# Kernel tuning notes

Hardware: AMD Instinct MI355X
Metric: run time of the kernel (lower is better)

## Reference

```python
import jax, jax.numpy as jnp
import numpy as np

L, S = 3, 5                 # A hierarchy layers, subsets per layer
CIN = COUT = 64
INTER = COUT // (S - 1)     # 16
BC = COUT // 4              # 16 channels per TCN branch
N, T, V = 128, 128, 25
KS = 5
DILS = (1, 2)
EPS = 1e-5


def setup_inputs() -> dict:
    key = jax.random.key(0)
    ks = jax.random.split(key, 22)
    rn = lambda i, shape, s=0.1: jax.random.normal(ks[i], shape, jnp.float32) * s
    g1 = lambda i, shape: 1.0 + jax.random.normal(ks[i], shape, jnp.float32) * 0.05
    return {
        'x':      jax.random.normal(ks[0], (N, CIN, T, V), jnp.float32),
        'PA':     rn(1, (L, S, V, V), 0.2),
        'gdw':    rn(2, (L, INTER, CIN)),
        'gdb':    rn(3, (L, INTER)),
        'gdg':    g1(4, (L, INTER)),
        'gdbt':   rn(5, (L, INTER)),
        'gsw':    rn(6, (L, S, INTER, INTER)),
        'gsb':    rn(7, (L, S, INTER)),
        'gsg':    g1(8, (L, S, INTER)),
        'gsbt':   rn(9, (L, S, INTER)),
        'gbng':   g1(10, (COUT,)),
        'gbnb':   rn(11, (COUT,)),
        'brw':    rn(12, (4, BC, COUT)),
        'brb':    rn(13, (4, BC)),
        'brg':    g1(14, (4, BC)),
        'brbt':   rn(15, (4, BC)),
        'tcw':    rn(16, (2, BC, BC, KS, 1)),
        'tcbias': rn(17, (2, BC)),
        'tcg':    g1(18, (2, BC)),
        'tcbt':   rn(19, (2, BC)),
        'mpg':    g1(20, (BC,)),
        'mpb':    rn(21, (BC,)),
    }


def _bn(x, g, b):
    # training-mode BatchNorm2d over (N, T, V) with biased variance
    m = x.mean(axis=(0, 2, 3), keepdims=True)
    v = ((x - m) ** 2).mean(axis=(0, 2, 3), keepdims=True)
    return (x - m) * jax.lax.rsqrt(v + EPS) * g[None, :, None, None] + b[None, :, None, None]


def _c1x1(x, w, b=None):
    y = jnp.einsum('nctv,oc->notv', x, w)
    return y if b is None else y + b[None, :, None, None]


def reference(x, PA, gdw, gdb, gdg, gdbt, gsw, gsb, gsg, gsbt, gbng, gbnb,
              brw, brb, brg, brbt, tcw, tcbias, tcg, tcbt, mpg, mpb):
    # ---- UbH_Gconv ----
    layer_outs = []
    for i in range(L):
        xd = jax.nn.relu(_bn(_c1x1(x, gdw[i], gdb[i]), gdg[i], gdbt[i]))
        ys = [
            _bn(_c1x1(jnp.einsum('nctu,vu->nctv', xd, PA[i, j]), gsw[i, j], gsb[i, j]),
                gsg[i, j], gsbt[i, j])
            for j in range(S)
        ]
        layer_outs.append(jnp.concatenate(ys, axis=1))      # [N, S*INTER, T, V]
    out = jnp.stack(layer_outs, axis=2)                     # [N, S*INTER, L, T, V]
    base = out[:, :INTER]                                   # subset-0 block
    new = out[:, INTER:] + jnp.tile(base, (1, S - 1, 1, 1, 1))
    new = new.sum(axis=2)                                   # sum over hierarchy layers -> [N, COUT, T, V]
    xg = jax.nn.relu(_bn(new, gbng, gbnb) + x)              # residual down is identity (CIN==COUT)

    # ---- MultiScale_TemporalConv (residual=False) ----
    branches = []
    for k, d in enumerate(DILS):
        y = jax.nn.relu(_bn(_c1x1(xg, brw[k], brb[k]), brg[k], brbt[k]))
        pad = (KS + (KS - 1) * (d - 1) - 1) // 2
        y = jax.lax.conv_general_dilated(
            y, tcw[k], window_strides=(1, 1), padding=((pad, pad), (0, 0)),
            rhs_dilation=(d, 1), dimension_numbers=('NCHW', 'OIHW', 'NCHW'))
        y = y + tcbias[k][None, :, None, None]
        branches.append(_bn(y, tcg[k], tcbt[k]))
    # maxpool branch
    y = jax.nn.relu(_bn(_c1x1(xg, brw[2], brb[2]), brg[2], brbt[2]))
    y = jax.lax.reduce_window(y, -jnp.inf, jax.lax.max, (1, 1, 3, 1), (1, 1, 1, 1),
                              ((0, 0), (0, 0), (1, 1), (0, 0)))
    branches.append(_bn(y, mpg, mpb))
    # plain 1x1 branch
    branches.append(_bn(_c1x1(xg, brw[3], brb[3]), brg[3], brbt[3]))

    t = jnp.concatenate(branches, axis=1)                   # [N, COUT, T, V]
    # unit residual is identity (CIN==COUT, stride==1)
    return jax.nn.relu(t + xg)
```

## Files before the change

kernel.cpp:

```cpp
#include <hip/hip_runtime.h>

#define N_ 128
#define T_ 128
#define V_ 25
#define TV 3200
#define LL 3
#define SS 5
#define II 16
#define EPSB 1e-5f
#define MCNT 409600.0f


__device__ __forceinline__ float2 bncoef(const float2* st, int slot, float g, float bt){
  float2 s = st[slot];
  float m  = s.x * (1.0f/MCNT);
  float var = s.y * (1.0f/MCNT) - m*m;
  float a = g * rsqrtf(var + EPSB);
  return make_float2(a, bt - m*a);
}

__global__ __launch_bounds__(256) void k1_conv_dw(
    const float* __restrict__ x, const float* __restrict__ gdw, const float* __restrict__ gdb,
    float* __restrict__ c1, float2* st)
{
  __shared__ float w[64*48];
  __shared__ float bias[48];
  __shared__ float bst[4][96];
  const int tid = threadIdx.x;
  for (int i = tid; i < 64*48; i += 256){ int c = i/48, o = i - c*48; w[i] = gdw[o*64 + c]; }
  if (tid < 48) bias[tid] = gdb[tid];
  __syncthreads();
  const int n = blockIdx.y;
  const int rem = blockIdx.x*256 + tid;
  const bool act = rem < TV;
  float acc[48];
  #pragma unroll
  for (int o = 0; o < 48; o++) acc[o] = act ? bias[o] : 0.f;
  const float* xp = x + (size_t)n*64*TV + rem;
  if (act){
    #pragma unroll 4
    for (int c = 0; c < 64; c++){
      float xv = xp[c*TV];
      const float4* w4 = (const float4*)&w[c*48];
      #pragma unroll
      for (int o4 = 0; o4 < 12; o4++){
        float4 ww = w4[o4];
        acc[o4*4+0] += ww.x*xv; acc[o4*4+1] += ww.y*xv;
        acc[o4*4+2] += ww.z*xv; acc[o4*4+3] += ww.w*xv;
      }
    }
    #pragma unroll
    for (int o = 0; o < 48; o++){
      int l = o >> 4, oi = o & 15;
      c1[(size_t)((l*N_+n)*II + oi)*TV + rem] = acc[o];
    }
  }
  const int wv = tid >> 6, lane = tid & 63;
  #pragma unroll
  for (int o = 0; o < 48; o++){
    float s = acc[o], q = acc[o]*acc[o];
    #pragma unroll
    for (int m = 32; m; m >>= 1){ s += __shfl_xor(s, m); q += __shfl_xor(q, m); }
    if (lane == 0){ bst[wv][2*o] = s; bst[wv][2*o+1] = q; }
  }
  __syncthreads();
  float* stf = (float*)st;
  if (tid < 96) unsafeAtomicAdd(stf + tid, bst[0][tid]+bst[1][tid]+bst[2][tid]+bst[3][tid]);
}

__global__ __launch_bounds__(256) void k2_spatial_stats(
    const float* __restrict__ c1, const float* __restrict__ PA,
    const float* __restrict__ gsw, const float* __restrict__ gsb,
    const float* __restrict__ gdg, const float* __restrict__ gdbt,
    float2* st)
{
  __shared__ float pa[5][25][28];
  __shared__ float gw[5][16][20];
  __shared__ float xdl[4][16][28];
  __shared__ float zz[4][25][20];
  __shared__ float cA[16], cB[16];
  __shared__ float bst[4][160];
  const int tid = threadIdx.x;
  const int l = blockIdx.z, n = blockIdx.y;
  for (int i = tid; i < 5*625; i += 256){ int j = i/625, r = i - j*625; pa[j][r/25][r%25] = PA[(l*5+j)*625 + r]; }
  for (int i = tid; i < 5*256; i += 256){ int j = i >> 8, r = i & 255; gw[j][r>>4][r&15] = gsw[(l*5+j)*256 + r]; }
  if (tid < 16){
    float2 ab = bncoef(st, l*16+tid, gdg[l*16+tid], gdbt[l*16+tid]);
    cA[tid] = ab.x; cB[tid] = ab.y;
  }
  __syncthreads();
  const int wv = tid >> 6, lane = tid & 63, oc = lane & 15, vg = lane >> 4;
  const int t = blockIdx.x*4 + wv;
  const float* c1p = c1 + (size_t)((l*N_+n)*II)*TV + t*25;
  for (int idx = lane; idx < 400; idx += 64){
    int c = idx/25, v = idx - c*25;
    float val = c1p[c*TV + v];
    xdl[wv][c][v] = fmaxf(cA[c]*val + cB[c], 0.f);
  }
  float xdr[25];
  {
    const float4* xr4 = (const float4*)&xdl[wv][oc][0];
    #pragma unroll
    for (int u4 = 0; u4 < 6; u4++){
      float4 x4 = xr4[u4];
      xdr[u4*4+0]=x4.x; xdr[u4*4+1]=x4.y; xdr[u4*4+2]=x4.z; xdr[u4*4+3]=x4.w;
    }
    xdr[24] = xdl[wv][oc][24];
  }
  #pragma unroll 1
  for (int j = 0; j < 5; j++){
    #pragma unroll
    for (int k = 0; k < 7; k++){
      int v = vg + 4*k;
      if (v < 25){
        const float4* p4 = (const float4*)&pa[j][v][0];
        float zv = 0.f;
        #pragma unroll
        for (int u4 = 0; u4 < 6; u4++){
          float4 pp = p4[u4];
          zv += xdr[u4*4+0]*pp.x + xdr[u4*4+1]*pp.y + xdr[u4*4+2]*pp.z + xdr[u4*4+3]*pp.w;
        }
        zv += xdr[24]*pa[j][v][24];
        zz[wv][v][oc] = zv;
      }
    }
    float gwr[16];
    {
      const float4* g4 = (const float4*)&gw[j][oc][0];
      #pragma unroll
      for (int c4 = 0; c4 < 4; c4++){
        float4 gg = g4[c4];
        gwr[c4*4+0]=gg.x; gwr[c4*4+1]=gg.y; gwr[c4*4+2]=gg.z; gwr[c4*4+3]=gg.w;
      }
    }
    const float bjo = gsb[(l*5+j)*16 + oc];
    float s = 0.f, q = 0.f;
    #pragma unroll
    for (int k = 0; k < 7; k++){
      int v = vg + 4*k;
      if (v < 25){
        const float4* z4 = (const float4*)&zz[wv][v][0];
        float cv = bjo;
        #pragma unroll
        for (int c4 = 0; c4 < 4; c4++){
          float4 zf = z4[c4];
          cv += gwr[c4*4+0]*zf.x + gwr[c4*4+1]*zf.y + gwr[c4*4+2]*zf.z + gwr[c4*4+3]*zf.w;
        }
        s += cv; q += cv*cv;
      }
    }
    s += __shfl_xor(s,16); s += __shfl_xor(s,32);
    q += __shfl_xor(q,16); q += __shfl_xor(q,32);
    if (vg == 0){ bst[wv][2*(j*16+oc)] = s; bst[wv][2*(j*16+oc)+1] = q; }
  }
  __syncthreads();
  float* stf = (float*)st;
  for (int i = tid; i < 160; i += 256)
    unsafeAtomicAdd(stf + 96 + l*160 + i, bst[0][i]+bst[1][i]+bst[2][i]+bst[3][i]);
}

__global__ __launch_bounds__(256) void k3_new(
    const float* __restrict__ c1, const float* __restrict__ PA,
    const float* __restrict__ gsw, const float* __restrict__ gsb,
    const float* __restrict__ gdg, const float* __restrict__ gdbt,
    const float* __restrict__ gsg, const float* __restrict__ gsbt,
    float2* st, float* __restrict__ newb)
{
  __shared__ float pa[5][25][28];
  __shared__ float gw[5][16][20];
  __shared__ float xdl[4][16][28];
  __shared__ float zz[4][25][20];
  __shared__ float cA[16], cB[16];
  __shared__ float c2A[5][16], c2B[5][16];
  __shared__ float bst[4][128];
  const int tid = threadIdx.x;
  const int n = blockIdx.y;
  const int wv = tid >> 6, lane = tid & 63, oc = lane & 15, vg = lane >> 4;
  const int t = blockIdx.x*4 + wv;
  float base[7], ac1[7], ac2[7], ac3[7], ac4[7];
  #pragma unroll
  for (int k = 0; k < 7; k++){ base[k]=0.f; ac1[k]=0.f; ac2[k]=0.f; ac3[k]=0.f; ac4[k]=0.f; }

  #pragma unroll 1
  for (int l = 0; l < 3; l++){
    __syncthreads();
    for (int i = tid; i < 5*625; i += 256){ int j = i/625, r = i - j*625; pa[j][r/25][r%25] = PA[(l*5+j)*625 + r]; }
    for (int i = tid; i < 5*256; i += 256){ int j = i >> 8, r = i & 255; gw[j][r>>4][r&15] = gsw[(l*5+j)*256 + r]; }
    if (tid < 16){
      float2 ab = bncoef(st, l*16+tid, gdg[l*16+tid], gdbt[l*16+tid]);
      cA[tid] = ab.x; cB[tid] = ab.y;
    }
    if (tid < 80){
      int j = tid >> 4, o = tid & 15;
      float2 ab = bncoef(st, 48 + (l*5+j)*16 + o, gsg[(l*5+j)*16+o], gsbt[(l*5+j)*16+o]);
      c2A[j][o] = ab.x; c2B[j][o] = ab.y;
    }
    __syncthreads();
    const float* c1p = c1 + (size_t)((l*N_+n)*II)*TV + t*25;
    for (int idx = lane; idx < 400; idx += 64){
      int c = idx/25, v = idx - c*25;
      float val = c1p[c*TV + v];
      xdl[wv][c][v] = fmaxf(cA[c]*val + cB[c], 0.f);
    }
    float xdr[25];
    {
      const float4* xr4 = (const float4*)&xdl[wv][oc][0];
      #pragma unroll
      for (int u4 = 0; u4 < 6; u4++){
        float4 x4 = xr4[u4];
        xdr[u4*4+0]=x4.x; xdr[u4*4+1]=x4.y; xdr[u4*4+2]=x4.z; xdr[u4*4+3]=x4.w;
      }
      xdr[24] = xdl[wv][oc][24];
    }
    #pragma unroll 1
    for (int j = 0; j < 5; j++){
      #pragma unroll
      for (int k = 0; k < 7; k++){
        int v = vg + 4*k;
        if (v < 25){
          const float4* p4 = (const float4*)&pa[j][v][0];
          float zv = 0.f;
          #pragma unroll
          for (int u4 = 0; u4 < 6; u4++){
            float4 pp = p4[u4];
            zv += xdr[u4*4+0]*pp.x + xdr[u4*4+1]*pp.y + xdr[u4*4+2]*pp.z + xdr[u4*4+3]*pp.w;
          }
          zv += xdr[24]*pa[j][v][24];
          zz[wv][v][oc] = zv;
        }
      }
      float gwr[16];
      {
        const float4* g4 = (const float4*)&gw[j][oc][0];
        #pragma unroll
        for (int c4 = 0; c4 < 4; c4++){
          float4 gg = g4[c4];
          gwr[c4*4+0]=gg.x; gwr[c4*4+1]=gg.y; gwr[c4*4+2]=gg.z; gwr[c4*4+3]=gg.w;
        }
      }
      const float bjo = gsb[(l*5+j)*16 + oc];
      const float a2 = c2A[j][oc], b2 = c2B[j][oc];
      float ybuf[7];
      #pragma unroll
      for (int k = 0; k < 7; k++){
        int v = vg + 4*k;
        ybuf[k] = 0.f;
        if (v < 25){
          const float4* z4 = (const float4*)&zz[wv][v][0];
          float cv = bjo;
          #pragma unroll
          for (int c4 = 0; c4 < 4; c4++){
            float4 zf = z4[c4];
            cv += gwr[c4*4+0]*zf.x + gwr[c4*4+1]*zf.y + gwr[c4*4+2]*zf.z + gwr[c4*4+3]*zf.w;
          }
          ybuf[k] = a2*cv + b2;
        }
      }
      if (j == 0){
        #pragma unroll
        for (int k = 0; k < 7; k++) base[k] += ybuf[k];
      } else if (j == 1){
        #pragma unroll
        for (int k = 0; k < 7; k++) ac1[k] += ybuf[k];
      } else if (j == 2){
        #pragma unroll
        for (int k = 0; k < 7; k++) ac2[k] += ybuf[k];
      } else if (j == 3){
        #pragma unroll
        for (int k = 0; k < 7; k++) ac3[k] += ybuf[k];
      } else {
        #pragma unroll
        for (int k = 0; k < 7; k++) ac4[k] += ybuf[k];
      }
    }
  }
  float* np = newb + (size_t)n*64*TV + t*25;
  float s0=0.f,q0=0.f,s1=0.f,q1=0.f,s2=0.f,q2=0.f,s3=0.f,q3=0.f;
  #pragma unroll
  for (int k = 0; k < 7; k++){
    int v = vg + 4*k;
    if (v < 25){
      float v0 = ac1[k] + base[k];
      float v1 = ac2[k] + base[k];
      float v2 = ac3[k] + base[k];
      float v3 = ac4[k] + base[k];
      np[(0*16+oc)*TV + v] = v0;
      np[(1*16+oc)*TV + v] = v1;
      np[(2*16+oc)*TV + v] = v2;
      np[(3*16+oc)*TV + v] = v3;
      s0 += v0; q0 += v0*v0;
      s1 += v1; q1 += v1*v1;
      s2 += v2; q2 += v2*v2;
      s3 += v3; q3 += v3*v3;
    }
  }
  s0 += __shfl_xor(s0,16); s0 += __shfl_xor(s0,32);
  q0 += __shfl_xor(q0,16); q0 += __shfl_xor(q0,32);
  s1 += __shfl_xor(s1,16); s1 += __shfl_xor(s1,32);
  q1 += __shfl_xor(q1,16); q1 += __shfl_xor(q1,32);
  s2 += __shfl_xor(s2,16); s2 += __shfl_xor(s2,32);
  q2 += __shfl_xor(q2,16); q2 += __shfl_xor(q2,32);
  s3 += __shfl_xor(s3,16); s3 += __shfl_xor(s3,32);
  q3 += __shfl_xor(q3,16); q3 += __shfl_xor(q3,32);
  if (vg == 0){
    bst[wv][2*(0*16+oc)] = s0; bst[wv][2*(0*16+oc)+1] = q0;
    bst[wv][2*(1*16+oc)] = s1; bst[wv][2*(1*16+oc)+1] = q1;
    bst[wv][2*(2*16+oc)] = s2; bst[wv][2*(2*16+oc)+1] = q2;
    bst[wv][2*(3*16+oc)] = s3; bst[wv][2*(3*16+oc)+1] = q3;
  }
  __syncthreads();
  float* stf = (float*)st;
  for (int i = tid; i < 128; i += 256)
    unsafeAtomicAdd(stf + 576 + i, bst[0][i]+bst[1][i]+bst[2][i]+bst[3][i]);
}

__global__ __launch_bounds__(256) void k4_xg_branches(
    const float* __restrict__ x, const float* __restrict__ newb,
    const float* __restrict__ gbng, const float* __restrict__ gbnb,
    const float* __restrict__ brw, const float* __restrict__ brb,
    float2* st, float* __restrict__ xg, float* __restrict__ y)
{
  __shared__ float w[64*64];
  __shared__ float cA[64], cB[64], bias[64];
  __shared__ float bst[4][128];
  const int tid = threadIdx.x;
  for (int i = tid; i < 4096; i += 256){ int c = i >> 6, ko = i & 63; w[i] = brw[ko*64 + c]; }
  if (tid < 64){
    float2 ab = bncoef(st, 288+tid, gbng[tid], gbnb[tid]);
    cA[tid] = ab.x; cB[tid] = ab.y; bias[tid] = brb[tid];
  }
  __syncthreads();
  const int n = blockIdx.y;
  const int rem = blockIdx.x*256 + tid;
  const bool act = rem < TV;
  const float* xp  = x    + (size_t)n*64*TV + rem;
  const float* npx = newb + (size_t)n*64*TV + rem;
  float*       xgp = xg   + (size_t)n*64*TV + rem;
  float xgv[64];
  #pragma unroll
  for (int c = 0; c < 64; c++){
    float v = 0.f;
    if (act){
      v = fmaxf(cA[c]*npx[c*TV] + cB[c] + xp[c*TV], 0.f);
      xgp[c*TV] = v;
    }
    xgv[c] = v;
  }
  const int wv = tid >> 6, lane = tid & 63;
  #pragma unroll
  for (int k = 0; k < 4; k++){
    float acc[16];
    #pragma unroll
    for (int o = 0; o < 16; o++) acc[o] = act ? bias[k*16+o] : 0.f;
    #pragma unroll
    for (int c = 0; c < 64; c++){
      float xv = xgv[c];
      const float4* w4 = (const float4*)&w[c*64 + k*16];
      #pragma unroll
      for (int o4 = 0; o4 < 4; o4++){
        float4 ww = w4[o4];
        acc[o4*4+0] += ww.x*xv; acc[o4*4+1] += ww.y*xv;
        acc[o4*4+2] += ww.z*xv; acc[o4*4+3] += ww.w*xv;
      }
    }
    if (act){
      float* yp = y + (size_t)((k*N_+n)*16)*TV + rem;
      #pragma unroll
      for (int o = 0; o < 16; o++) yp[o*TV] = acc[o];
    }
    #pragma unroll
    for (int o = 0; o < 16; o++){
      float s = acc[o], q = acc[o]*acc[o];
      #pragma unroll
      for (int m = 32; m; m >>= 1){ s += __shfl_xor(s, m); q += __shfl_xor(q, m); }
      if (lane == 0){ bst[wv][2*(k*16+o)] = s; bst[wv][2*(k*16+o)+1] = q; }
    }
  }
  __syncthreads();
  float* stf = (float*)st;
  for (int i = tid; i < 128; i += 256)
    unsafeAtomicAdd(stf + 704 + i, bst[0][i]+bst[1][i]+bst[2][i]+bst[3][i]);
}

__global__ __launch_bounds__(256) void k5_temporal(
    const float* __restrict__ y, const float* __restrict__ tcw, const float* __restrict__ tcbias,
    const float* __restrict__ brg, const float* __restrict__ brbt,
    float2* st, float* __restrict__ tp)
{
  __shared__ float wt[2*16*5*16];
  __shared__ float cAy[48], cBy[48];
  __shared__ float bst[4][96];
  const int tid = threadIdx.x;
  for (int i = tid; i < 2560; i += 256){
    int k = i/1280, r = i - k*1280, c = r/80, r2 = r - c*80, ks = r2 >> 4, o = r2 & 15;
    wt[i] = tcw[((k*16+o)*16 + c)*5 + ks];
  }
  if (tid < 48){
    float2 ab = bncoef(st, 352+tid, brg[tid], brbt[tid]);
    cAy[tid] = ab.x; cBy[tid] = ab.y;
  }
  __syncthreads();
  const int n = blockIdx.y;
  const int rem = blockIdx.x*256 + tid;
  const bool act = rem < TV;
  const int t = rem/25, v = rem - t*25;
  const int wv = tid >> 6, lane = tid & 63;
  #pragma unroll
  for (int k = 0; k < 2; k++){
    const int d = k + 1;
    float acc[16];
    #pragma unroll
    for (int o = 0; o < 16; o++) acc[o] = act ? tcbias[k*16+o] : 0.f;
    if (act){
      const float* yp = y + (size_t)((k*N_+n)*16)*TV;
      #pragma unroll
      for (int ks = 0; ks < 5; ks++){
        int ttt = t + d*(ks-2);
        if (ttt >= 0 && ttt < T_){
          int off = ttt*25 + v;
          #pragma unroll
          for (int c = 0; c < 16; c++){
            float val = fmaxf(cAy[k*16+c]*yp[c*TV + off] + cBy[k*16+c], 0.f);
            const float4* w4 = (const float4*)&wt[((k*16+c)*5 + ks)*16];
            #pragma unroll
            for (int o4 = 0; o4 < 4; o4++){
              float4 ww = w4[o4];
              acc[o4*4+0] += ww.x*val; acc[o4*4+1] += ww.y*val;
              acc[o4*4+2] += ww.z*val; acc[o4*4+3] += ww.w*val;
            }
          }
        }
      }
      float* op = tp + (size_t)k*6553600 + (size_t)(n*16)*TV + rem;
      #pragma unroll
      for (int o = 0; o < 16; o++) op[o*TV] = acc[o];
    }
    #pragma unroll
    for (int o = 0; o < 16; o++){
      float s = acc[o], q = acc[o]*acc[o];
      #pragma unroll
      for (int m = 32; m; m >>= 1){ s += __shfl_xor(s, m); q += __shfl_xor(q, m); }
      if (lane == 0){ bst[wv][2*(k*16+o)] = s; bst[wv][2*(k*16+o)+1] = q; }
    }
  }
  {
    float mx[16];
    #pragma unroll
    for (int o = 0; o < 16; o++) mx[o] = -1e30f;
    if (act){
      const float* yp = y + (size_t)((2*N_+n)*16)*TV;
      #pragma unroll
      for (int dt = -1; dt <= 1; dt++){
        int ttt = t + dt;
        if (ttt >= 0 && ttt < T_){
          int off = ttt*25 + v;
          #pragma unroll
          for (int o = 0; o < 16; o++){
            float val = fmaxf(cAy[32+o]*yp[o*TV + off] + cBy[32+o], 0.f);
            mx[o] = fmaxf(mx[o], val);
          }
        }
      }
      float* op = tp + (size_t)2*6553600 + (size_t)(n*16)*TV + rem;
      #pragma unroll
      for (int o = 0; o < 16; o++) op[o*TV] = mx[o];
    } else {
      #pragma unroll
      for (int o = 0; o < 16; o++) mx[o] = 0.f;
    }
    #pragma unroll
    for (int o = 0; o < 16; o++){
      float s = mx[o], q = mx[o]*mx[o];
      #pragma unroll
      for (int m = 32; m; m >>= 1){ s += __shfl_xor(s, m); q += __shfl_xor(q, m); }
      if (lane == 0){ bst[wv][64 + 2*o] = s; bst[wv][64 + 2*o + 1] = q; }
    }
  }
  __syncthreads();
  float* stf = (float*)st;
  for (int i = tid; i < 96; i += 256)
    unsafeAtomicAdd(stf + 832 + i, bst[0][i]+bst[1][i]+bst[2][i]+bst[3][i]);
}

__global__ __launch_bounds__(256) void k6_final(
    const float* __restrict__ tp, const float* __restrict__ y, const float* __restrict__ xg,
    const float* __restrict__ tcg, const float* __restrict__ tcbt,
    const float* __restrict__ mpg, const float* __restrict__ mpb,
    const float* __restrict__ brg, const float* __restrict__ brbt,
    const float2* __restrict__ st, float* __restrict__ out)
{
  __shared__ float cA[64], cB[64];
  const int tid = threadIdx.x;
  if (tid < 64){
    int o = tid & 15;
    float2 ab;
    if (tid < 32)      ab = bncoef(st, 416 + tid, tcg[tid], tcbt[tid]);
    else if (tid < 48) ab = bncoef(st, 448 + o, mpg[o], mpb[o]);
    else               ab = bncoef(st, 400 + o, brg[48+o], brbt[48+o]);
    cA[tid] = ab.x; cB[tid] = ab.y;
  }
  __syncthreads();
  const int n = blockIdx.y;
  const int rem = blockIdx.x*256 + tid;
  if (rem >= TV) return;
  const float* xgp = xg + (size_t)n*64*TV + rem;
  float* op = out + (size_t)n*64*TV + rem;
  #pragma unroll
  for (int ch = 0; ch < 64; ch++){
    int o = ch & 15;
    float sv;
    if (ch < 48) sv = tp[(size_t)(ch>>4)*6553600 + (size_t)(n*16+o)*TV + rem];
    else         sv = y[(size_t)((3*N_+n)*16 + o)*TV + rem];
    float val = cA[ch]*sv + cB[ch] + xgp[ch*TV];
    op[ch*TV] = fmaxf(val, 0.f);
  }
}

extern "C" void kernel_launch(void* const* d_in, const int* in_sizes, int n_in,
                              void* d_out, int out_size, void* d_ws, size_t ws_size,
                              hipStream_t stream) {
  (void)in_sizes; (void)n_in; (void)out_size; (void)ws_size;
  const float* x    = (const float*)d_in[0];
  const float* PA   = (const float*)d_in[1];
  const float* gdw  = (const float*)d_in[2];
  const float* gdb  = (const float*)d_in[3];
  const float* gdg  = (const float*)d_in[4];
  const float* gdbt = (const float*)d_in[5];
  const float* gsw  = (const float*)d_in[6];
  const float* gsb  = (const float*)d_in[7];
  const float* gsg  = (const float*)d_in[8];
  const float* gsbt = (const float*)d_in[9];
  const float* gbng = (const float*)d_in[10];
  const float* gbnb = (const float*)d_in[11];
  const float* brw  = (const float*)d_in[12];
  const float* brb  = (const float*)d_in[13];
  const float* brg  = (const float*)d_in[14];
  const float* brbt = (const float*)d_in[15];
  const float* tcw  = (const float*)d_in[16];
  const float* tcbias=(const float*)d_in[17];
  const float* tcg  = (const float*)d_in[18];
  const float* tcbt = (const float*)d_in[19];
  const float* mpg  = (const float*)d_in[20];
  const float* mpb  = (const float*)d_in[21];

  char* ws = (char*)d_ws;
  float2* st  = (float2*)ws;
  float* c1   = (float*)(ws + 4096);
  float* tp   = c1;
  float* newb = (float*)(ws + 4096 + 78643200);
  float* xg   = (float*)(ws + 4096 + 78643200 + 104857600);
  float* y    = (float*)(ws + 4096 + 78643200 + 209715200);

  hipMemsetAsync(st, 0, 4096, stream);
  dim3 b(256);
  k1_conv_dw     <<<dim3(13,128),   b, 0, stream>>>(x, gdw, gdb, c1, st);
  k2_spatial_stats<<<dim3(32,128,3), b, 0, stream>>>(c1, PA, gsw, gsb, gdg, gdbt, st);
  k3_new         <<<dim3(32,128),   b, 0, stream>>>(c1, PA, gsw, gsb, gdg, gdbt, gsg, gsbt, st, newb);
  k4_xg_branches <<<dim3(13,128),   b, 0, stream>>>(x, newb, gbng, gbnb, brw, brb, st, xg, y);
  k5_temporal    <<<dim3(13,128),   b, 0, stream>>>(y, tcw, tcbias, brg, brbt, st, tp);
  k6_final       <<<dim3(13,128),   b, 0, stream>>>(tp, y, xg, tcg, tcbt, mpg, mpb, brg, brbt, st, (float*)d_out);
}
```

Measured before the change: 1.399 ms.

## Remap spatial kernels so PA rows are wave-uniform scalar loads, dropping LDS staging

```diff
diff --git a/kernel.cpp b/kernel.cpp
--- a/kernel.cpp
+++ b/kernel.cpp
@@ -74,84 +74,71 @@
     const float* __restrict__ gdg, const float* __restrict__ gdbt,
     float2* st)
 {
-  __shared__ float pa[5][25][28];
-  __shared__ float gw[5][16][20];
-  __shared__ float xdl[4][16][28];
-  __shared__ float zz[4][25][20];
-  __shared__ float cA[16], cB[16];
+  __shared__ float zz[4][25][16];
   __shared__ float bst[4][160];
   const int tid = threadIdx.x;
   const int l = blockIdx.z, n = blockIdx.y;
-  for (int i = tid; i < 5*625; i += 256){ int j = i/625, r = i - j*625; pa[j][r/25][r%25] = PA[(l*5+j)*625 + r]; }
-  for (int i = tid; i < 5*256; i += 256){ int j = i >> 8, r = i & 255; gw[j][r>>4][r&15] = gsw[(l*5+j)*256 + r]; }
-  if (tid < 16){
-    float2 ab = bncoef(st, l*16+tid, gdg[l*16+tid], gdbt[l*16+tid]);
-    cA[tid] = ab.x; cB[tid] = ab.y;
-  }
-  __syncthreads();
-  const int wv = tid >> 6, lane = tid & 63, oc = lane & 15, vg = lane >> 4;
-  const int t = blockIdx.x*4 + wv;
-  const float* c1p = c1 + (size_t)((l*N_+n)*II)*TV + t*25;
-  for (int idx = lane; idx < 400; idx += 64){
-    int c = idx/25, v = idx - c*25;
-    float val = c1p[c*TV + v];
-    xdl[wv][c][v] = fmaxf(cA[c]*val + cB[c], 0.f);
+  const int wu = __builtin_amdgcn_readfirstlane(tid >> 6);
+  const int lane = tid & 63;
+  const int t2 = lane >> 4, oc = lane & 15;
+  const int t = blockIdx.x*4 + t2;
+  float cAr, cBr;
+  {
+    float2 s = st[l*16+oc];
+    float m = s.x*(1.f/MCNT), var = s.y*(1.f/MCNT) - m*m;
+    cAr = gdg[l*16+oc]*rsqrtf(var+EPSB);
+    cBr = gdbt[l*16+oc] - m*cAr;
   }
   float xdr[25];
   {
-    const float4* xr4 = (const float4*)&xdl[wv][oc][0];
-    #pragma unroll
-    for (int u4 = 0; u4 < 6; u4++){
-      float4 x4 = xr4[u4];
-      xdr[u4*4+0]=x4.x; xdr[u4*4+1]=x4.y; xdr[u4*4+2]=x4.z; xdr[u4*4+3]=x4.w;
-    }
-    xdr[24] = xdl[wv][oc][24];
+    const float* c1p = c1 + ((size_t)((l*N_+n)*II + oc))*TV + t*25;
+    #pragma unroll
+    for (int u = 0; u < 25; u++) xdr[u] = fmaxf(cAr*c1p[u] + cBr, 0.f);
   }
   #pragma unroll 1
   for (int j = 0; j < 5; j++){
-    #pragma unroll
-    for (int k = 0; k < 7; k++){
-      int v = vg + 4*k;
-      if (v < 25){
-        const float4* p4 = (const float4*)&pa[j][v][0];
-        float zv = 0.f;
-        #pragma unroll
-        for (int u4 = 0; u4 < 6; u4++){
-          float4 pp = p4[u4];
-          zv += xdr[u4*4+0]*pp.x + xdr[u4*4+1]*pp.y + xdr[u4*4+2]*pp.z + xdr[u4*4+3]*pp.w;
+    const float* paJ = PA + (size_t)(l*5+j)*625;
+    const float* gwp = gsw + ((size_t)((l*5+j)*16 + oc))*16;
+    float gwr[16];
+    #pragma unroll
+    for (int c4 = 0; c4 < 4; c4++){
+      float4 g4 = *(const float4*)(gwp + 4*c4);
+      gwr[4*c4+0]=g4.x; gwr[4*c4+1]=g4.y; gwr[4*c4+2]=g4.z; gwr[4*c4+3]=g4.w;
+    }
+    const float bjo = gsb[(l*5+j)*16 + oc];
+    float ssum = 0.f, sq = 0.f;
+    #pragma unroll
+    for (int i = 0; i < 7; i++){
+      const int vreal = wu + 4*i;
+      const int v = vreal < 25 ? vreal : 24;
+      const float* par = paJ + v*25;
+      float pan[25];
+      #pragma unroll
+      for (int u = 0; u < 25; u++) pan[u] = par[u];
+      if (vreal < 25){
+        float z0 = xdr[0]*pan[0], z1 = xdr[1]*pan[1], z2 = xdr[2]*pan[2], z3 = xdr[3]*pan[3];
+        #pragma unroll
+        for (int u = 4; u < 24; u += 4){
+          z0 += xdr[u+0]*pan[u+0];
+          z1 += xdr[u+1]*pan[u+1];
+          z2 += xdr[u+2]*pan[u+2];
+          z3 += xdr[u+3]*pan[u+3];
         }
-        zv += xdr[24]*pa[j][v][24];
-        zz[wv][v][oc] = zv;
-      }
-    }
-    float gwr[16];
-    {
-      const float4* g4 = (const float4*)&gw[j][oc][0];
-      #pragma unroll
-      for (int c4 = 0; c4 < 4; c4++){
-        float4 gg = g4[c4];
-        gwr[c4*4+0]=gg.x; gwr[c4*4+1]=gg.y; gwr[c4*4+2]=gg.z; gwr[c4*4+3]=gg.w;
-      }
-    }
-    const float bjo = gsb[(l*5+j)*16 + oc];
-    float s = 0.f, q = 0.f;
-    #pragma unroll
-    for (int k = 0; k < 7; k++){
-      int v = vg + 4*k;
-      if (v < 25){
-        const float4* z4 = (const float4*)&zz[wv][v][0];
-        float cv = bjo;
-        #pragma unroll
-        for (int c4 = 0; c4 < 4; c4++){
-          float4 zf = z4[c4];
-          cv += gwr[c4*4+0]*zf.x + gwr[c4*4+1]*zf.y + gwr[c4*4+2]*zf.z + gwr[c4*4+3]*zf.w;
-        }
-        s += cv; q += cv*cv;
-      }
-    }
-    s += __shfl_xor(s,16); s += __shfl_xor(s,32);
-    q += __shfl_xor(q,16); q += __shfl_xor(q,32);
-    if (vg == 0){ bst[wv][2*(j*16+oc)] = s; bst[wv][2*(j*16+oc)+1] = q; }
+        z0 += xdr[24]*pan[24];
+        zz[t2][v][oc] = (z0+z1)+(z2+z3);
+        const float4* zr = (const float4*)&zz[t2][v][0];
+        float4 za = zr[0], zb = zr[1], zc = zr[2], zd = zr[3];
+        float d0 = gwr[0]*za.x + gwr[1]*za.y + gwr[2]*za.z + gwr[3]*za.w;
+        float d1 = gwr[4]*zb.x + gwr[5]*zb.y + gwr[6]*zb.z + gwr[7]*zb.w;
+        float d2 = gwr[8]*zc.x + gwr[9]*zc.y + gwr[10]*zc.z + gwr[11]*zc.w;
+        float d3 = gwr[12]*zd.x + gwr[13]*zd.y + gwr[14]*zd.z + gwr[15]*zd.w;
+        float cv = bjo + ((d0+d1)+(d2+d3));
+        ssum += cv; sq += cv*cv;
+      }
+    }
+    ssum += __shfl_xor(ssum,16); ssum += __shfl_xor(ssum,32);
+    sq   += __shfl_xor(sq,16);   sq   += __shfl_xor(sq,32);
+    if (t2 == 0){ bst[wu][2*(j*16+oc)] = ssum; bst[wu][2*(j*16+oc)+1] = sq; }
   }
   __syncthreads();
   float* stf = (float*)st;
@@ -166,124 +153,110 @@
     const float* __restrict__ gsg, const float* __restrict__ gsbt,
     float2* st, float* __restrict__ newb)
 {
-  __shared__ float pa[5][25][28];
-  __shared__ float gw[5][16][20];
-  __shared__ float xdl[4][16][28];
-  __shared__ float zz[4][25][20];
-  __shared__ float cA[16], cB[16];
-  __shared__ float c2A[5][16], c2B[5][16];
+  __shared__ float zz[4][25][16];
   __shared__ float bst[4][128];
   const int tid = threadIdx.x;
   const int n = blockIdx.y;
-  const int wv = tid >> 6, lane = tid & 63, oc = lane & 15, vg = lane >> 4;
-  const int t = blockIdx.x*4 + wv;
+  const int wu = __builtin_amdgcn_readfirstlane(tid >> 6);
+  const int lane = tid & 63;
+  const int t2 = lane >> 4, oc = lane & 15;
+  const int t = blockIdx.x*4 + t2;
   float base[7], ac1[7], ac2[7], ac3[7], ac4[7];
   #pragma unroll
-  for (int k = 0; k < 7; k++){ base[k]=0.f; ac1[k]=0.f; ac2[k]=0.f; ac3[k]=0.f; ac4[k]=0.f; }
+  for (int i = 0; i < 7; i++){ base[i]=0.f; ac1[i]=0.f; ac2[i]=0.f; ac3[i]=0.f; ac4[i]=0.f; }
 
   #pragma unroll 1
   for (int l = 0; l < 3; l++){
-    __syncthreads();
-    for (int i = tid; i < 5*625; i += 256){ int j = i/625, r = i - j*625; pa[j][r/25][r%25] = PA[(l*5+j)*625 + r]; }
-    for (int i = tid; i < 5*256; i += 256){ int j = i >> 8, r = i & 255; gw[j][r>>4][r&15] = gsw[(l*5+j)*256 + r]; }
-    if (tid < 16){
-      float2 ab = bncoef(st, l*16+tid, gdg[l*16+tid], gdbt[l*16+tid]);
-      cA[tid] = ab.x; cB[tid] = ab.y;
-    }
-    if (tid < 80){
-      int j = tid >> 4, o = tid & 15;
-      float2 ab = bncoef(st, 48 + (l*5+j)*16 + o, gsg[(l*5+j)*16+o], gsbt[(l*5+j)*16+o]);
-      c2A[j][o] = ab.x; c2B[j][o] = ab.y;
-    }
-    __syncthreads();
-    const float* c1p = c1 + (size_t)((l*N_+n)*II)*TV + t*25;
-    for (int idx = lane; idx < 400; idx += 64){
-      int c = idx/25, v = idx - c*25;
-      float val = c1p[c*TV + v];
-      xdl[wv][c][v] = fmaxf(cA[c]*val + cB[c], 0.f);
+    float cAr, cBr;
+    {
+      float2 s = st[l*16+oc];
+      float m = s.x*(1.f/MCNT), var = s.y*(1.f/MCNT) - m*m;
+      cAr = gdg[l*16+oc]*rsqrtf(var+EPSB);
+      cBr = gdbt[l*16+oc] - m*cAr;
     }
     float xdr[25];
     {
-      const float4* xr4 = (const float4*)&xdl[wv][oc][0];
-      #pragma unroll
-      for (int u4 = 0; u4 < 6; u4++){
-        float4 x4 = xr4[u4];
-        xdr[u4*4+0]=x4.x; xdr[u4*4+1]=x4.y; xdr[u4*4+2]=x4.z; xdr[u4*4+3]=x4.w;
-      }
-      xdr[24] = xdl[wv][oc][24];
+      const float* c1p = c1 + ((size_t)((l*N_+n)*II + oc))*TV + t*25;
+      #pragma unroll
+      for (int u = 0; u < 25; u++) xdr[u] = fmaxf(cAr*c1p[u] + cBr, 0.f);
     }
     #pragma unroll 1
     for (int j = 0; j < 5; j++){
-      #pragma unroll
-      for (int k = 0; k < 7; k++){
-        int v = vg + 4*k;
-        if (v < 25){
-          const float4* p4 = (const float4*)&pa[j][v][0];
-          float zv = 0.f;
+      const float* paJ = PA + (size_t)(l*5+j)*625;
+      const float* gwp = gsw + ((size_t)((l*5+j)*16 + oc))*16;
+      float gwr[16];
+      #pragma unroll
+      for (int c4 = 0; c4 < 4; c4++){
+        float4 g4 = *(const float4*)(gwp + 4*c4);
+        gwr[4*c4+0]=g4.x; gwr[4*c4+1]=g4.y; gwr[4*c4+2]=g4.z; gwr[4*c4+3]=g4.w;
+      }
+      const float bjo = gsb[(l*5+j)*16 + oc];
+      float a2, b2;
+      {
+        int slot = 48 + (l*5+j)*16 + oc;
+        float2 s = st[slot];
+        float m = s.x*(1.f/MCNT), var = s.y*(1.f/MCNT) - m*m;
+        a2 = gsg[(l*5+j)*16+oc]*rsqrtf(var+EPSB);
+        b2 = gsbt[(l*5+j)*16+oc] - m*a2;
+      }
+      float yb_[7];
+      #pragma unroll
+      for (int i = 0; i < 7; i++){
+        const int vreal = wu + 4*i;
+        const int v = vreal < 25 ? vreal : 24;
+        const float* par = paJ + v*25;
+        float pan[25];
+        #pragma unroll
+        for (int u = 0; u < 25; u++) pan[u] = par[u];
+        yb_[i] = 0.f;
+        if (vreal < 25){
+          float z0 = xdr[0]*pan[0], z1 = xdr[1]*pan[1], z2 = xdr[2]*pan[2], z3 = xdr[3]*pan[3];
           #pragma unroll
-          for (int u4 = 0; u4 < 6; u4++){
-            float4 pp = p4[u4];
-            zv += xdr[u4*4+0]*pp.x + xdr[u4*4+1]*pp.y + xdr[u4*4+2]*pp.z + xdr[u4*4+3]*pp.w;
+          for (int u = 4; u < 24; u += 4){
+            z0 += xdr[u+0]*pan[u+0];
+            z1 += xdr[u+1]*pan[u+1];
+            z2 += xdr[u+2]*pan[u+2];
+            z3 += xdr[u+3]*pan[u+3];
           }
-          zv += xdr[24]*pa[j][v][24];
-          zz[wv][v][oc] = zv;
+          z0 += xdr[24]*pan[24];
+          zz[t2][v][oc] = (z0+z1)+(z2+z3);
+          const float4* zr = (const float4*)&zz[t2][v][0];
+          float4 za = zr[0], zb = zr[1], zc = zr[2], zd = zr[3];
+          float d0 = gwr[0]*za.x + gwr[1]*za.y + gwr[2]*za.z + gwr[3]*za.w;
+          float d1 = gwr[4]*zb.x + gwr[5]*zb.y + gwr[6]*zb.z + gwr[7]*zb.w;
+          float d2 = gwr[8]*zc.x + gwr[9]*zc.y + gwr[10]*zc.z + gwr[11]*zc.w;
+          float d3 = gwr[12]*zd.x + gwr[13]*zd.y + gwr[14]*zd.z + gwr[15]*zd.w;
+          yb_[i] = a2*(bjo + ((d0+d1)+(d2+d3))) + b2;
         }
       }
-      float gwr[16];
-      {
-        const float4* g4 = (const float4*)&gw[j][oc][0];
-        #pragma unroll
-        for (int c4 = 0; c4 < 4; c4++){
-          float4 gg = g4[c4];
-          gwr[c4*4+0]=gg.x; gwr[c4*4+1]=gg.y; gwr[c4*4+2]=gg.z; gwr[c4*4+3]=gg.w;
-        }
-      }
-      const float bjo = gsb[(l*5+j)*16 + oc];
-      const float a2 = c2A[j][oc], b2 = c2B[j][oc];
-      float ybuf[7];
-      #pragma unroll
-      for (int k = 0; k < 7; k++){
-        int v = vg + 4*k;
-        ybuf[k] = 0.f;
-        if (v < 25){
-          const float4* z4 = (const float4*)&zz[wv][v][0];
-          float cv = bjo;
-          #pragma unroll
-          for (int c4 = 0; c4 < 4; c4++){
-            float4 zf = z4[c4];
-            cv += gwr[c4*4+0]*zf.x + gwr[c4*4+1]*zf.y + gwr[c4*4+2]*zf.z + gwr[c4*4+3]*zf.w;
-          }
-          ybuf[k] = a2*cv + b2;
-        }
-      }
       if (j == 0){
         #pragma unroll
-        for (int k = 0; k < 7; k++) base[k] += ybuf[k];
+        for (int i = 0; i < 7; i++) base[i] += yb_[i];
       } else if (j == 1){
         #pragma unroll
-        for (int k = 0; k < 7; k++) ac1[k] += ybuf[k];
+        for (int i = 0; i < 7; i++) ac1[i] += yb_[i];
       } else if (j == 2){
         #pragma unroll
-        for (int k = 0; k < 7; k++) ac2[k] += ybuf[k];
+        for (int i = 0; i < 7; i++) ac2[i] += yb_[i];
       } else if (j == 3){
         #pragma unroll
-        for (int k = 0; k < 7; k++) ac3[k] += ybuf[k];
+        for (int i = 0; i < 7; i++) ac3[i] += yb_[i];
       } else {
         #pragma unroll
-        for (int k = 0; k < 7; k++) ac4[k] += ybuf[k];
+        for (int i = 0; i < 7; i++) ac4[i] += yb_[i];
       }
     }
   }
   float* np = newb + (size_t)n*64*TV + t*25;
   float s0=0.f,q0=0.f,s1=0.f,q1=0.f,s2=0.f,q2=0.f,s3=0.f,q3=0.f;
   #pragma unroll
-  for (int k = 0; k < 7; k++){
-    int v = vg + 4*k;
+  for (int i = 0; i < 7; i++){
+    const int v = wu + 4*i;
     if (v < 25){
-      float v0 = ac1[k] + base[k];
-      float v1 = ac2[k] + base[k];
-      float v2 = ac3[k] + base[k];
-      float v3 = ac4[k] + base[k];
+      float v0 = ac1[i] + base[i];
+      float v1 = ac2[i] + base[i];
+      float v2 = ac3[i] + base[i];
+      float v3 = ac4[i] + base[i];
       np[(0*16+oc)*TV + v] = v0;
       np[(1*16+oc)*TV + v] = v1;
       np[(2*16+oc)*TV + v] = v2;
@@ -302,11 +275,11 @@
   q2 += __shfl_xor(q2,16); q2 += __shfl_xor(q2,32);
   s3 += __shfl_xor(s3,16); s3 += __shfl_xor(s3,32);
   q3 += __shfl_xor(q3,16); q3 += __shfl_xor(q3,32);
-  if (vg == 0){
-    bst[wv][2*(0*16+oc)] = s0; bst[wv][2*(0*16+oc)+1] = q0;
-    bst[wv][2*(1*16+oc)] = s1; bst[wv][2*(1*16+oc)+1] = q1;
-    bst[wv][2*(2*16+oc)] = s2; bst[wv][2*(2*16+oc)+1] = q2;
-    bst[wv][2*(3*16+oc)] = s3; bst[wv][2*(3*16+oc)+1] = q3;
+  if (t2 == 0){
+    bst[wu][2*(0*16+oc)] = s0; bst[wu][2*(0*16+oc)+1] = q0;
+    bst[wu][2*(1*16+oc)] = s1; bst[wu][2*(1*16+oc)+1] = q1;
+    bst[wu][2*(2*16+oc)] = s2; bst[wu][2*(2*16+oc)+1] = q2;
+    bst[wu][2*(3*16+oc)] = s3; bst[wu][2*(3*16+oc)+1] = q3;
   }
   __syncthreads();
   float* stf = (float*)st;
```

After: 1.420 ms. About the same (+1.6%).
